# Performance work log

Hardware: AMD Instinct MI355X
Metric: run time of the kernel (lower is better)

The kernel has to match this reference:

```python
import jax, jax.numpy as jnp
import numpy as np


def setup_inputs() -> dict:
    key = jax.random.key(0)
    k1, k2, k3 = jax.random.split(key, 3)
    worker_num, task_num, edge_type, ability_num = 2048, 2048, 16, 64
    # inputs stacks worker feature rows [:worker_num, :ability_num]
    # and task label-probability rows [worker_num:, :edge_type]
    inputs = jax.random.uniform(k1, (worker_num + task_num, ability_num), dtype=jnp.float32)
    W = jax.random.normal(k2, (ability_num, 1), dtype=jnp.float32)
    b = jax.random.normal(k3, (1,), dtype=jnp.float32)
    return {
        "inputs": inputs,
        "W": W,
        "b": b,
        "worker_num": worker_num,
        "task_num": task_num,
        "edge_type": edge_type,
        "ability_num": ability_num,
    }


def reference(inputs, W, b, worker_num, task_num, edge_type, ability_num):
    # Worker features: [Wn, A]; task label distributions tau: [T, L]
    worker_feature = inputs[:worker_num, :ability_num]
    tau = inputs[worker_num:, :edge_type]
    # prob_part1 = sigmoid(w_i . W + b): per-worker correctness probability, [Wn, 1]
    p1 = jax.nn.sigmoid(worker_feature @ W + b)
    # prob_part2: remaining mass spread over the other (L-1) labels, [Wn, 1]
    p2 = (1.0 - p1) / jnp.float32(edge_type - 1)
    # P[i,j,l] = p1[i]^tau[j,l] * p2[i]^(1 - tau[j,l])  -> [Wn, T, L]
    p1 = p1[:, :, None]  # [Wn, 1, 1]
    p2 = p2[:, :, None]
    tau_b = tau[None, :, :]  # [1, T, L]
    P = jnp.power(p1, tau_b) * jnp.power(p2, 1.0 - tau_b)
    return P
```

## Files before the change

kernel.cpp:

```cpp
#include <hip/hip_runtime.h>

#define WORKERS 2048
#define TASKS   2048
#define ETYPE   16
#define ABIL    64

#define F4_PER_WORKER  8192
#define ITERS          32

typedef float f4 __attribute__((ext_vector_type(4)));

__global__ void __launch_bounds__(256)
fused_kernel(const float* __restrict__ inputs,
             const float* __restrict__ W,
             const float* __restrict__ b,
             f4* __restrict__ out) {
    const int w = blockIdx.x;

    const f4* row = reinterpret_cast<const f4*>(inputs + (size_t)w * ABIL);
    const f4* Wv  = reinterpret_cast<const f4*>(W);
    float acc = 0.0f;
#pragma unroll
    for (int k = 0; k < ABIL / 4; ++k) {
        f4 x  = row[k];
        f4 wv = Wv[k];
        acc = fmaf(x.x, wv.x, acc);
        acc = fmaf(x.y, wv.y, acc);
        acc = fmaf(x.z, wv.z, acc);
        acc = fmaf(x.w, wv.w, acc);
    }
    acc += b[0];
    const float LOG2E = 1.4426950408889634f;
    float e  = __builtin_amdgcn_exp2f(-acc * LOG2E);
    float p1 = 1.0f / (1.0f + e);
    float p2 = (1.0f - p1) * (1.0f / (ETYPE - 1));
    const float a = __builtin_amdgcn_logf(p1);
    const float c = __builtin_amdgcn_logf(p2);

    const int base = w * F4_PER_WORKER + (int)threadIdx.x;
#pragma unroll 4
    for (int it = 0; it < ITERS; ++it) {
        const int i    = base + it * 256;
        const int rem4 = i & (F4_PER_WORKER - 1);
        const int t    = rem4 >> 2;
        const int e0   = (rem4 & 3) * 4;
        const f4 tau = *reinterpret_cast<const f4*>(
            inputs + (size_t)(WORKERS + t) * ABIL + e0);
        f4 r;
        r.x = __builtin_amdgcn_exp2f(fmaf(tau.x, a, (1.0f - tau.x) * c));
        r.y = __builtin_amdgcn_exp2f(fmaf(tau.y, a, (1.0f - tau.y) * c));
        r.z = __builtin_amdgcn_exp2f(fmaf(tau.z, a, (1.0f - tau.z) * c));
        r.w = __builtin_amdgcn_exp2f(fmaf(tau.w, a, (1.0f - tau.w) * c));
        __builtin_nontemporal_store(r, &out[i]);
    }
}

extern "C" void kernel_launch(void* const* d_in, const int* in_sizes, int n_in,
                              void* d_out, int out_size, void* d_ws, size_t ws_size,
                              hipStream_t stream) {
    const float* inputs = (const float*)d_in[0];
    const float* W      = (const float*)d_in[1];
    const float* b      = (const float*)d_in[2];

    fused_kernel<<<WORKERS, 256, 0, stream>>>(inputs, W, b, (f4*)d_out);
}
```

Before: 57.36 us.

## Retile grid so each block holds tau in registers across 32 workers

The grid is restructured so each block covers a 256-float4 slice of tasks by 32 workers. Each thread loads its tau vector once and reuses it across 32 worker rows. The per-worker sigmoid/log coefficients are computed cooperatively with shuffle reductions and shared through LDS. The nontemporal store hint is also replaced with a regular store, which may change cache behavior on the bandwidth-bound output write.

```diff
diff --git a/kernel.cpp b/kernel.cpp
--- a/kernel.cpp
+++ b/kernel.cpp
@@ -5,53 +5,72 @@
 #define ETYPE   16
 #define ABIL    64
 
-#define F4_PER_WORKER  8192
-#define ITERS          32
+#define F4_PER_WORKER 8192
+#define TE_BLOCKS     32
+#define W_PER_BLOCK   32
+#define NBLOCKS ((WORKERS / W_PER_BLOCK) * TE_BLOCKS)
 
 typedef float f4 __attribute__((ext_vector_type(4)));
 
 __global__ void __launch_bounds__(256)
-fused_kernel(const float* __restrict__ inputs,
-             const float* __restrict__ W,
-             const float* __restrict__ b,
-             f4* __restrict__ out) {
-    const int w = blockIdx.x;
+stream_kernel(const float* __restrict__ inputs,
+              const float* __restrict__ W,
+              const float* __restrict__ bb,
+              f4* __restrict__ out) {
+    __shared__ float sA[W_PER_BLOCK];
+    __shared__ float sC[W_PER_BLOCK];
 
-    const f4* row = reinterpret_cast<const f4*>(inputs + (size_t)w * ABIL);
-    const f4* Wv  = reinterpret_cast<const f4*>(W);
-    float acc = 0.0f;
-#pragma unroll
-    for (int k = 0; k < ABIL / 4; ++k) {
-        f4 x  = row[k];
-        f4 wv = Wv[k];
-        acc = fmaf(x.x, wv.x, acc);
-        acc = fmaf(x.y, wv.y, acc);
-        acc = fmaf(x.z, wv.z, acc);
-        acc = fmaf(x.w, wv.w, acc);
+    const int tid    = threadIdx.x;
+    const int blk    = blockIdx.x;
+    const int te_grp = blk & (TE_BLOCKS - 1);
+    const int wgrp   = blk >> 5;
+    const int w0     = wgrp * W_PER_BLOCK;
+
+    const int te  = te_grp * 256 + tid;
+    const int t   = te >> 2;
+    const int e0  = (te & 3) * 4;
+    const f4 tau  = *reinterpret_cast<const f4*>(
+        inputs + (size_t)(WORKERS + t) * ABIL + e0);
+
+    {
+        const int lw = tid >> 3;
+        const int ch = tid & 7;
+        const f4* rv = reinterpret_cast<const f4*>(
+            inputs + (size_t)(w0 + lw) * ABIL + ch * 8);
+        const f4* Wv = reinterpret_cast<const f4*>(W + ch * 8);
+        f4 x0 = rv[0], x1 = rv[1];
+        f4 y0 = Wv[0], y1 = Wv[1];
+        float acc = 0.0f;
+        acc = fmaf(x0.x, y0.x, acc); acc = fmaf(x0.y, y0.y, acc);
+        acc = fmaf(x0.z, y0.z, acc); acc = fmaf(x0.w, y0.w, acc);
+        acc = fmaf(x1.x, y1.x, acc); acc = fmaf(x1.y, y1.y, acc);
+        acc = fmaf(x1.z, y1.z, acc); acc = fmaf(x1.w, y1.w, acc);
+        acc += __shfl_xor(acc, 1, 64);
+        acc += __shfl_xor(acc, 2, 64);
+        acc += __shfl_xor(acc, 4, 64);
+        if (ch == 0) {
+            acc += bb[0];
+            const float LOG2E = 1.4426950408889634f;
+            float e  = __builtin_amdgcn_exp2f(-acc * LOG2E);
+            float p1 = 1.0f / (1.0f + e);
+            float p2 = (1.0f - p1) * (1.0f / (ETYPE - 1));
+            sA[lw] = __builtin_amdgcn_logf(p1);
+            sC[lw] = __builtin_amdgcn_logf(p2);
+        }
     }
-    acc += b[0];
-    const float LOG2E = 1.4426950408889634f;
-    float e  = __builtin_amdgcn_exp2f(-acc * LOG2E);
-    float p1 = 1.0f / (1.0f + e);
-    float p2 = (1.0f - p1) * (1.0f / (ETYPE - 1));
-    const float a = __builtin_amdgcn_logf(p1);
-    const float c = __builtin_amdgcn_logf(p2);
+    __syncthreads();
 
-    const int base = w * F4_PER_WORKER + (int)threadIdx.x;
-#pragma unroll 4
-    for (int it = 0; it < ITERS; ++it) {
-        const int i    = base + it * 256;
-        const int rem4 = i & (F4_PER_WORKER - 1);
-        const int t    = rem4 >> 2;
-        const int e0   = (rem4 & 3) * 4;
-        const f4 tau = *reinterpret_cast<const f4*>(
-            inputs + (size_t)(WORKERS + t) * ABIL + e0);
+    f4* outp = out + (size_t)w0 * F4_PER_WORKER + te;
+#pragma unroll 8
+    for (int lw = 0; lw < W_PER_BLOCK; ++lw) {
+        const float a = sA[lw];
+        const float c = sC[lw];
         f4 r;
         r.x = __builtin_amdgcn_exp2f(fmaf(tau.x, a, (1.0f - tau.x) * c));
         r.y = __builtin_amdgcn_exp2f(fmaf(tau.y, a, (1.0f - tau.y) * c));
         r.z = __builtin_amdgcn_exp2f(fmaf(tau.z, a, (1.0f - tau.z) * c));
         r.w = __builtin_amdgcn_exp2f(fmaf(tau.w, a, (1.0f - tau.w) * c));
-        __builtin_nontemporal_store(r, &out[i]);
+        outp[(size_t)lw * F4_PER_WORKER] = r;
     }
 }
 
@@ -62,5 +81,5 @@
     const float* W      = (const float*)d_in[1];
     const float* b      = (const float*)d_in[2];
 
-    fused_kernel<<<WORKERS, 256, 0, stream>>>(inputs, W, b, (f4*)d_out);
+    stream_kernel<<<NBLOCKS, 256, 0, stream>>>(inputs, W, b, (f4*)d_out);
 }
```

Measured after the change: 47.62 us. 17.0% less time.
